# Kernel tuning notes

Hardware: AMD Instinct MI355X
Metric: run time of the kernel (lower is better)

Reference implementation:

```python
import jax, jax.numpy as jnp
import numpy as np

N_NODES = 10000
N_REL = 200
DIM = 128          # rank * 2
REL_DIM = 128
VIS_DIM = 512
TXT_DIM = 768
N_EDGES = 320000


def _glorot(key, shape):
    fan_in, fan_out = shape[1], shape[0]
    lim = (6.0 / (fan_in + fan_out)) ** 0.5
    return jax.random.uniform(key, shape, jnp.float32, -lim, lim)


def setup_inputs() -> dict:
    key = jax.random.key(0)
    ks = jax.random.split(key, 24)
    inp = {}
    inp['x'] = jax.random.randint(ks[0], (1024, 3), 0, N_NODES)
    inp['edge_index'] = jax.random.randint(ks[1], (2, N_EDGES), 0, N_NODES)
    inp['edge_type'] = jax.random.randint(ks[2], (N_EDGES,), 0, N_REL)
    inp['visual'] = jax.random.normal(ks[3], (N_NODES, VIS_DIM), jnp.float32)
    inp['textual'] = jax.random.normal(ks[4], (N_NODES, TXT_DIM), jnp.float32)
    # embeddings (scaled by 0.001 as in torch init)
    inp['structural_emb'] = jax.random.normal(ks[5], (N_NODES, DIM), jnp.float32) * 0.001
    inp['relation_emb'] = jax.random.normal(ks[6], (N_REL, REL_DIM), jnp.float32) * 0.001
    # three KBGAT convs: w1 [out, 2*in+rel], b1 [out], w2 [1, out]
    cat = 2 * DIM + REL_DIM
    for i, tag in enumerate(['s', 'v', 't']):
        inp[f'W1_{tag}'] = _glorot(ks[7 + 3 * i], (DIM, cat))
        inp[f'b1_{tag}'] = jnp.zeros((DIM,), jnp.float32)
        inp[f'w2_{tag}'] = _glorot(ks[8 + 3 * i], (1, DIM))
    # modality projections
    inp['Wv'] = _glorot(ks[16], (DIM, VIS_DIM))
    inp['bv'] = jnp.zeros((DIM,), jnp.float32)
    inp['Wt'] = _glorot(ks[17], (DIM, TXT_DIM))
    inp['bt'] = jnp.zeros((DIM,), jnp.float32)
    inp['alpha'] = jnp.float32(0.1)
    inp['gamma'] = jnp.float32(0.8)
    return inp


def kbgat_conv(feat, rel_emb, src, dst, edge_type, W1, b1, w2):
    # gather per-edge embeddings: x_i = target, x_j = source (PyG default flow)
    triple = jnp.concatenate([feat[dst], feat[src], rel_emb[edge_type]], axis=1)  # [E, 2*D+R]
    c = triple @ W1.T + b1                                   # [E, D]
    b = jax.nn.leaky_relu(c @ w2[0])                         # [E]
    # segment softmax over destination nodes
    m = jax.ops.segment_max(b, dst, num_segments=N_NODES)
    e = jnp.exp(b - m[dst])
    z = jax.ops.segment_sum(e, dst, num_segments=N_NODES)
    attn = e / z[dst]                                        # [E]
    agg = jax.ops.segment_sum(c * attn[:, None], dst, num_segments=N_NODES)  # [N, D]
    return jax.nn.leaky_relu(agg)


def reference(x, edge_index, edge_type, visual, textual, structural_emb, relation_emb,
              W1_s, b1_s, w2_s, W1_v, b1_v, w2_v, W1_t, b1_t, w2_t,
              Wv, bv, Wt, bt, alpha, gamma):
    src, dst = edge_index[0], edge_index[1]
    h_s = kbgat_conv(structural_emb, relation_emb, src, dst, edge_type, W1_s, b1_s, w2_s)
    vf = visual @ Wv.T + bv
    h_v = kbgat_conv(vf, relation_emb, src, dst, edge_type, W1_v, b1_v, w2_v)
    tf = textual @ Wt.T + bt
    h_t = kbgat_conv(tf, relation_emb, src, dst, edge_type, W1_t, b1_t, w2_t)
    return (1.0 - alpha - gamma) * h_s + alpha * h_v + gamma * h_t
```

## Files before the change

### kernel.cpp

```cpp
#include <hip/hip_runtime.h>
#include <hip/hip_bf16.h>

typedef unsigned short u16;
typedef unsigned int u32;
typedef unsigned long long u64;
typedef __bf16 bf16x8 __attribute__((ext_vector_type(8)));
typedef float f32x4 __attribute__((ext_vector_type(4)));

#define DIM 128

__device__ __forceinline__ u16 f2bf_rne(float x) {
  u32 u = __float_as_uint(x);
  return (u16)((u + 0x7fffu + ((u >> 16) & 1u)) >> 16);
}
__device__ __forceinline__ u32 packbf2(float x, float y) {
  return (u32)f2bf_rne(x) | ((u32)f2bf_rne(y) << 16);
}
__device__ __forceinline__ float lrelu(float x) { return x > 0.f ? x : 0.01f * x; }
__device__ __forceinline__ int iclamp(int v, int hi) { return v < 0 ? 0 : (v >= hi ? hi - 1 : v); }
__device__ __forceinline__ float sane(float x) { return (x == x) ? x : 0.f; }

__device__ __forceinline__ float wred_max(float v) {
  #pragma unroll
  for (int o = 32; o > 0; o >>= 1) v = fmaxf(v, __shfl_xor(v, o, 64));
  return v;
}
__device__ __forceinline__ float wred_sum(float v) {
  #pragma unroll
  for (int o = 32; o > 0; o >>= 1) v += __shfl_xor(v, o, 64);
  return v;
}

struct PrepAllArgs {
  const float* W1[3]; const float* Wmod[3]; int K[3]; u16* Wc[3];
  const float* rel; const float* b1[3]; const float* bmod[3]; const float* w2[3];
  u16* PrAll; float* qr[3]; int NR;
  const int* dst; int* cnt; int* rank; int E; int N;
  int wc2End; int wc1End; int wc0End; int nCompute; int totB;
};
struct MainArgs {
  const float* A[3]; const u16* B[3]; const float* w2[3];
  u16* PdAll; u16* PsAll; float* qd[3]; float* qs[3];
  int M; int K[3]; int tilesPerM; int nGemm; int totB;
  const int* dst; const int* src; const int* etyp;
  const int* offs; const int* rank; u32* sortedST;
  int E; int NR;
};
struct AgArgs {
  const u32* sortedST; const int* offs;
  const float* qd[3]; const float* qs[3]; const float* qr[3];
  const u16* PdAll; const u16* PsAll; const u16* PrAll;
  const float* alphaP; const float* gammaP;
  float* outp; int N; int NR; int E;
};

__global__ __launch_bounds__(256) void fused_prep(PrepAllArgs a) {
  __shared__ float relL[2][128];
  __shared__ float bmL[128];
  __shared__ float qpr[4];
  int b = blockIdx.x, tid = threadIdx.x;
  long nC = a.nCompute, tot = a.totB;
  int cprev = (int)((long)b * nC / tot);
  int cnext = (int)(((long)b + 1) * nC / tot);
  if (cnext == cprev) {
    int e0 = (b - cprev) * 1024 + tid;
    #pragma unroll
    for (int i = 0; i < 4; ++i) {
      int e = e0 + i * 256;
      if (e < a.E) {
        int d = a.dst[e];
        if (d >= 0 && d < a.N) a.rank[e] = atomicAdd(&a.cnt[d], 1);
      }
    }
    return;
  }
  int c = cprev;
  if (c < a.wc0End) {
    int m, loc;
    if (c < a.wc2End)      { m = 2; loc = c; }
    else if (c < a.wc1End) { m = 1; loc = c - a.wc2End; }
    else                   { m = 0; loc = c - a.wc1End; }
    int og = loc & 31, kb = loc >> 5;
    int o0 = og * 8;
    int k = (kb << 8) + tid;
    int K = a.K[m];
    if (k < K) {
      int halfsel = (o0 >= 128) ? 128 : 0;
      int oo0 = o0 & 127;
      const float* W1 = a.W1[m];
      const float* Wm = a.Wmod[m];
      float acc[8];
      if (Wm == nullptr) {
        #pragma unroll
        for (int u = 0; u < 8; ++u)
          acc[u] = W1[(oo0 + u) * 384 + halfsel + k];
      } else {
        #pragma unroll
        for (int u = 0; u < 8; ++u) acc[u] = 0.f;
        const float* wmk = Wm + k;
        const float* w1b = W1 + (size_t)oo0 * 384 + halfsel;
        for (int i = 0; i < 128; i += 8) {
          float wm[8];
          #pragma unroll
          for (int j = 0; j < 8; ++j)
            wm[j] = wmk[(size_t)(i + j) * K];
          #pragma unroll
          for (int j = 0; j < 8; ++j) {
            #pragma unroll
            for (int u = 0; u < 8; ++u)
              acc[u] = fmaf(w1b[u * 384 + i + j], wm[j], acc[u]);
          }
        }
      }
      #pragma unroll
      for (int u = 0; u < 8; ++u) {
        int o = o0 + u;
        a.Wc[m][((size_t)(k >> 5) * 256 + o) * 32 + (k & 31)] = f2bf_rne(acc[u]);
      }
    }
  } else {
    int idx = c - a.wc0End;
    int NRpair = (a.NR + 1) >> 1;
    int m = idx / NRpair;
    if (m > 2) return;
    int rp = idx - m * NRpair;
    int r0 = rp * 2;
    {
      int ro = tid >> 7, ii = tid & 127;
      int rr = r0 + ro;
      relL[ro][ii] = (rr < a.NR) ? a.rel[rr * 128 + ii] : 0.f;
    }
    const float* bmod = a.bmod[m];
    if (tid < 128) bmL[tid] = (bmod != nullptr) ? bmod[tid] : 0.f;
    __syncthreads();
    int lane = tid & 63, wv = tid >> 6;
    int rsel = wv >> 1;
    int obase = (wv & 1) * 64;
    int r = r0 + rsel;
    bool rok = (r < a.NR);
    const float* W1 = a.W1[m];
    const float* b1 = a.b1[m];
    const float* w2 = a.w2[m];
    bool hasbm = (bmod != nullptr);
    float rl0 = relL[rsel][lane], rl1 = relL[rsel][64 + lane];
    float bm0 = bmL[lane], bm1 = bmL[64 + lane];
    float qacc = 0.f;
    for (int oo = 0; oo < 64; oo += 4) {
      float s[4];
      #pragma unroll
      for (int u = 0; u < 4; ++u) {
        const float* row = W1 + (obase + oo + u) * 384;
        float v = row[256 + lane] * rl0 + row[320 + lane] * rl1;
        if (hasbm)
          v += (row[lane] + row[128 + lane]) * bm0 +
               (row[64 + lane] + row[192 + lane]) * bm1;
        s[u] = v;
      }
      #pragma unroll
      for (int off2 = 32; off2 > 0; off2 >>= 1) {
        #pragma unroll
        for (int u = 0; u < 4; ++u) s[u] += __shfl_xor(s[u], off2, 64);
      }
      u16 pk[4];
      #pragma unroll
      for (int u = 0; u < 4; ++u) {
        int o = obase + oo + u;
        float totv = s[u] + b1[o];
        pk[u] = f2bf_rne(totv);
        qacc += totv * w2[o];
      }
      if (rok && lane == 0) {
        u16* dstp = a.PrAll + (size_t)r * 384 + m * 128 + obase + oo;
        *reinterpret_cast<u64*>(dstp) =
            (u64)pk[0] | ((u64)pk[1] << 16) | ((u64)pk[2] << 32) | ((u64)pk[3] << 48);
      }
    }
    if (lane == 0) qpr[wv] = qacc;
    __syncthreads();
    if (tid < 2) {
      int rr = r0 + tid;
      if (rr < a.NR) a.qr[m][rr] = sane(qpr[tid * 2] + qpr[tid * 2 + 1]);
    }
  }
}

__global__ __launch_bounds__(1024) void scan_k(const int* __restrict__ cnt,
                                               int* __restrict__ offs, int N) {
  __shared__ int sums[1024];
  int t = threadIdx.x;
  int chunk = (N + 1023) >> 10;
  int base = t * chunk;
  int s = 0;
  for (int i = 0; i < chunk; ++i) { int idx = base + i; if (idx < N) s += cnt[idx]; }
  sums[t] = s;
  __syncthreads();
  for (int off = 1; off < 1024; off <<= 1) {
    int v = (t >= off) ? sums[t - off] : 0;
    __syncthreads();
    sums[t] += v;
    __syncthreads();
  }
  int prefix = (t > 0) ? sums[t - 1] : 0;
  for (int i = 0; i < chunk; ++i) {
    int idx = base + i;
    if (idx < N) { offs[idx] = prefix; prefix += cnt[idx]; }
  }
  if (t == 1023) offs[N] = sums[1023];
}

__device__ __forceinline__ void gemm_epilogue(const MainArgs& g, int m, int row0,
                                              f32x4 (&acc)[2][4], float (*qpart)[32]) {
  int tid = threadIdx.x;
  int lane = tid & 63, wv = tid >> 6;
  int quad = lane >> 4, l16 = lane & 15;
  int M = g.M;
  const float* w2 = g.w2[m];
  u16* PdAll = g.PdAll;
  u16* PsAll = g.PsAll;
  float w2c[4];
  #pragma unroll
  for (int t = 0; t < 4; ++t) w2c[t] = w2[(wv & 1) * 64 + t * 16 + l16];

  #pragma unroll
  for (int rg = 0; rg < 2; ++rg) {
    float part[4];
    #pragma unroll
    for (int r = 0; r < 4; ++r) {
      int rr = row0 + rg * 16 + quad * 4 + r;
      bool ok = rr < M;
      float qp = 0.f;
      #pragma unroll
      for (int t = 0; t < 4; ++t) {
        int cc = (wv & 1) * 64 + t * 16 + l16;
        if (ok) {
          if (wv < 2) PdAll[(size_t)rr * 384 + m * 128 + cc] = f2bf_rne(acc[rg][t][r]);
          else        PsAll[(size_t)rr * 384 + m * 128 + cc] = f2bf_rne(acc[rg][t][r]);
        }
        qp += acc[rg][t][r] * w2c[t];
      }
      #pragma unroll
      for (int mk = 1; mk < 16; mk <<= 1) qp += __shfl_xor(qp, mk, 64);
      part[r] = qp;
    }
    if (l16 == 0) {
      #pragma unroll
      for (int r = 0; r < 4; ++r) qpart[wv][rg * 16 + quad * 4 + r] = part[r];
    }
  }
  __syncthreads();
  if (tid < 64) {
    int row = tid & 31;
    int half = tid >> 5;
    int rr = row0 + row;
    if (rr < M) {
      if (half == 0) g.qd[m][rr] = sane(qpart[0][row] + qpart[1][row]);
      else           g.qs[m][rr] = sane(qpart[2][row] + qpart[3][row]);
    }
  }
}

template<int NT>
__device__ __forceinline__ void gemm_exact(const MainArgs& g, int m, int tile,
                                           u16* Als, float (*qpart)[32]) {
  constexpr int H = (NT + 1) / 2;
  const int M = g.M;
  int tid = threadIdx.x;
  int lane = tid & 63, wv = tid >> 6;
  int quad = lane >> 4, l16 = lane & 15;
  int row0 = tile * 32;
  int srow = tid >> 3;
  int tk4 = (tid & 7) * 4;
  int srsw = srow & 3;
  int wg = tk4 >> 3;
  int wrem = tk4 & 7;
  int grow = row0 + srow;
  if (grow >= M) grow = M - 1;
  const float* Ag = g.A[m] + (size_t)grow * (NT * 32);

  float4 vreg[H];
  #pragma unroll
  for (int i = 0; i < H; ++i)
    vreg[i] = *reinterpret_cast<const float4*>(Ag + tk4 + i * 32);
  #pragma unroll
  for (int i = 0; i < H; ++i) {
    int gidx = wg ^ srsw ^ (i & 3);
    u32* dp = reinterpret_cast<u32*>(&Als[((i * 32 + srow) * 32) + (gidx << 3) + wrem]);
    dp[0] = packbf2(vreg[i].x, vreg[i].y);
    dp[1] = packbf2(vreg[i].z, vreg[i].w);
  }
  #pragma unroll
  for (int i = H; i < NT; ++i)
    vreg[i - H] = *reinterpret_cast<const float4*>(Ag + tk4 + i * 32);
  #pragma unroll
  for (int i = H; i < NT; ++i) {
    int gidx = wg ^ srsw ^ (i & 3);
    u32* dp = reinterpret_cast<u32*>(&Als[((i * 32 + srow) * 32) + (gidx << 3) + wrem]);
    dp[0] = packbf2(vreg[i - H].x, vreg[i - H].y);
    dp[1] = packbf2(vreg[i - H].z, vreg[i - H].w);
  }
  __syncthreads();

  const u16* Bpg = g.B[m] + (size_t)(wv * 64 + l16) * 32 + quad * 8;
  f32x4 acc[2][4];
  #pragma unroll
  for (int rg = 0; rg < 2; ++rg)
    #pragma unroll
    for (int t = 0; t < 4; ++t) acc[rg][t] = (f32x4){0.f, 0.f, 0.f, 0.f};

  #pragma unroll
  for (int kb = 0; kb < NT; ++kb) {
    const u16* bp = Bpg + (size_t)kb * 8192;
    bf16x8 b0 = *reinterpret_cast<const bf16x8*>(bp);
    bf16x8 b1 = *reinterpret_cast<const bf16x8*>(bp + 512);
    bf16x8 b2 = *reinterpret_cast<const bf16x8*>(bp + 1024);
    bf16x8 b3 = *reinterpret_cast<const bf16x8*>(bp + 1536);
    int gsw = (quad ^ (l16 & 3) ^ (kb & 3)) << 3;
    #pragma unroll
    for (int rg = 0; rg < 2; ++rg) {
      bf16x8 av = *reinterpret_cast<const bf16x8*>(
          &Als[(kb * 32 + rg * 16 + l16) * 32 + gsw]);
      acc[rg][0] = __builtin_amdgcn_mfma_f32_16x16x32_bf16(av, b0, acc[rg][0], 0, 0, 0);
      acc[rg][1] = __builtin_amdgcn_mfma_f32_16x16x32_bf16(av, b1, acc[rg][1], 0, 0, 0);
      acc[rg][2] = __builtin_amdgcn_mfma_f32_16x16x32_bf16(av, b2, acc[rg][2], 0, 0, 0);
      acc[rg][3] = __builtin_amdgcn_mfma_f32_16x16x32_bf16(av, b3, acc[rg][3], 0, 0, 0);
    }
  }
  gemm_epilogue(g, m, row0, acc, qpart);
}

__device__ void gemm_generic(const MainArgs& g, int m, int tile,
                             u16* Als, float (*qpart)[32]) {
  const int M = g.M, K = g.K[m];
  int nt = K >> 5;
  int tid = threadIdx.x;
  int lane = tid & 63, wv = tid >> 6;
  int quad = lane >> 4, l16 = lane & 15;
  int row0 = tile * 32;
  int srow = tid >> 3;
  int tk4 = (tid & 7) * 4;
  int srsw = srow & 3;
  int wg = tk4 >> 3;
  int wrem = tk4 & 7;
  int grow = row0 + srow;
  if (grow >= M) grow = M - 1;
  const float* Ag = g.A[m] + (size_t)grow * K;
  const u16* Bpg = g.B[m] + (size_t)(wv * 64 + l16) * 32 + quad * 8;

  f32x4 acc[2][4];
  #pragma unroll
  for (int rg = 0; rg < 2; ++rg)
    #pragma unroll
    for (int t = 0; t < 4; ++t) acc[rg][t] = (f32x4){0.f, 0.f, 0.f, 0.f};

  for (int c0 = 0; c0 < nt; c0 += 24) {
    int kc = nt - c0; if (kc > 24) kc = 24;
    __syncthreads();
    for (int i = 0; i < kc; ++i) {
      int kg = (c0 + i) * 32 + tk4;
      if (kg + 3 < K) {
        float4 v = *reinterpret_cast<const float4*>(Ag + kg);
        int gidx = wg ^ srsw ^ (i & 3);
        u32* dp = reinterpret_cast<u32*>(&Als[((i * 32 + srow) * 32) + (gidx << 3) + wrem]);
        dp[0] = packbf2(v.x, v.y);
        dp[1] = packbf2(v.z, v.w);
      }
    }
    __syncthreads();
    for (int kb = 0; kb < kc; ++kb) {
      const u16* bp = Bpg + (size_t)(c0 + kb) * 8192;
      bf16x8 b0 = *reinterpret_cast<const bf16x8*>(bp);
      bf16x8 b1 = *reinterpret_cast<const bf16x8*>(bp + 512);
      bf16x8 b2 = *reinterpret_cast<const bf16x8*>(bp + 1024);
      bf16x8 b3 = *reinterpret_cast<const bf16x8*>(bp + 1536);
      int gsw = (quad ^ (l16 & 3) ^ (kb & 3)) << 3;
      #pragma unroll
      for (int rg = 0; rg < 2; ++rg) {
        bf16x8 av = *reinterpret_cast<const bf16x8*>(
            &Als[(kb * 32 + rg * 16 + l16) * 32 + gsw]);
        acc[rg][0] = __builtin_amdgcn_mfma_f32_16x16x32_bf16(av, b0, acc[rg][0], 0, 0, 0);
        acc[rg][1] = __builtin_amdgcn_mfma_f32_16x16x32_bf16(av, b1, acc[rg][1], 0, 0, 0);
        acc[rg][2] = __builtin_amdgcn_mfma_f32_16x16x32_bf16(av, b2, acc[rg][2], 0, 0, 0);
        acc[rg][3] = __builtin_amdgcn_mfma_f32_16x16x32_bf16(av, b3, acc[rg][3], 0, 0, 0);
      }
    }
  }
  gemm_epilogue(g, m, row0, acc, qpart);
}

__global__ __launch_bounds__(256) void fused_main(MainArgs g) {
  __shared__ __align__(16) u16 Als[24 * 32 * 32];
  __shared__ float qpart[4][32];
  int b = blockIdx.x;
  long nG = g.nGemm, tot = g.totB;
  int gprev = (int)((long)b * nG / tot);
  int gnext = (int)(((long)b + 1) * nG / tot);
  if (gnext == gprev) {
    int h = b - gprev;
    int e = h * 256 + threadIdx.x;
    if (e < g.E) {
      int d = g.dst[e];
      if (d >= 0 && d < g.M) {
        int pos = g.offs[d] + g.rank[e];
        if (pos >= 0 && pos < g.E) {
          u32 s = (u32)iclamp(g.src[e], g.M);
          u32 t = (u32)iclamp(g.etyp[e], g.NR);
          g.sortedST[pos] = (t << 16) | s;
        }
      }
    }
    return;
  }
  int fb = gprev;
  int tpm = g.tilesPerM;
  int m, tile;
  if (fb < tpm)            { m = 2; tile = fb; }
  else if (fb < 2 * tpm)   { m = 1; tile = fb - tpm; }
  else                     { m = 0; tile = fb - 2 * tpm; }

  int K = g.K[m];
  if (K == 768)      gemm_exact<24>(g, m, tile, Als, qpart);
  else if (K == 512) gemm_exact<16>(g, m, tile, Als, qpart);
  else if (K == 128) gemm_exact<4>(g, m, tile, Als, qpart);
  else               gemm_generic(g, m, tile, Als, qpart);
}

__global__ __launch_bounds__(256) void aggregate_all(AgArgs a) {
  int n = blockIdx.x * 4 + (threadIdx.x >> 6);
  if (n >= a.N) return;
  int lane = threadIdx.x & 63;
  int E = a.E;
  int eb = a.offs[n], ee = a.offs[n + 1];
  if (eb < 0) eb = 0;
  if (eb > E) eb = E;
  if (ee < eb) ee = eb;
  if (ee > E) ee = E;
  int En = ee - eb;

  float al = a.alphaP[0];
  if (!(al > 0.f && al < 1.f)) al = 0.1f;
  float ga = a.gammaP[0];
  if (!(ga > 0.f && ga < 1.f)) ga = 0.8f;
  float coef[3] = {1.f - al - ga, al, ga};

  float qdn[3];
  #pragma unroll
  for (int m = 0; m < 3; ++m) qdn[m] = sane(a.qd[m][n]);

  const u16* PsAll = a.PsAll;
  const u16* PrAll = a.PrAll;
  int dlo = 2 * lane;

  float rm[3] = {-1e30f, -1e30f, -1e30f};
  float z[3] = {0.f, 0.f, 0.f};
  float a0[3] = {0.f, 0.f, 0.f};
  float a1[3] = {0.f, 0.f, 0.f};
  for (int c0 = 0; c0 < En; c0 += 64) {
    int cn = min(64, En - c0);
    u32 stp = 0;
    float bm[3] = {-1e30f, -1e30f, -1e30f};
    if (lane < cn) {
      stp = a.sortedST[eb + c0 + lane];
      int s = (int)(stp & 0xffffu);
      int t = (int)(stp >> 16);
      #pragma unroll
      for (int m = 0; m < 3; ++m)
        bm[m] = lrelu(qdn[m] + a.qs[m][s] + a.qr[m][t]);
    }
    float wr[3];
    #pragma unroll
    for (int m = 0; m < 3; ++m) {
      float cm = wred_max(bm[m]);
      float nm = fmaxf(rm[m], cm);
      float sc = __expf(fmaxf(rm[m] - nm, -80.f));
      z[m] *= sc; a0[m] *= sc; a1[m] *= sc;
      rm[m] = nm;
      wr[m] = (lane < cn) ? __expf(fmaxf(bm[m] - nm, -80.f)) : 0.f;
      z[m] += wr[m];
    }

    int cnR = (cn + 3) & ~3;
    for (int j = 0; j < cnR; j += 4) {
      u32 stj[4];
      float wj[4][3];
      #pragma unroll
      for (int u = 0; u < 4; ++u) {
        stj[u] = __shfl(stp, j + u, 64);
        wj[u][0] = __shfl(wr[0], j + u, 64);
        wj[u][1] = __shfl(wr[1], j + u, 64);
        wj[u][2] = __shfl(wr[2], j + u, 64);
      }
      u32 pu[4][3], ru[4][3];
      #pragma unroll
      for (int u = 0; u < 4; ++u) {
        const u16* ps = PsAll + (size_t)(stj[u] & 0xffffu) * 384 + dlo;
        const u16* pr = PrAll + (size_t)(stj[u] >> 16) * 384 + dlo;
        #pragma unroll
        for (int m = 0; m < 3; ++m) {
          pu[u][m] = *reinterpret_cast<const u32*>(ps + m * 128);
          ru[u][m] = *reinterpret_cast<const u32*>(pr + m * 128);
        }
      }
      #pragma unroll
      for (int u = 0; u < 4; ++u) {
        #pragma unroll
        for (int m = 0; m < 3; ++m) {
          float ps0 = __uint_as_float(pu[u][m] << 16);
          float ps1 = __uint_as_float(pu[u][m] & 0xffff0000u);
          float pr0 = __uint_as_float(ru[u][m] << 16);
          float pr1 = __uint_as_float(ru[u][m] & 0xffff0000u);
          a0[m] = fmaf(wj[u][m], ps0 + pr0, a0[m]);
          a1[m] = fmaf(wj[u][m], ps1 + pr1, a1[m]);
        }
      }
    }
  }
  #pragma unroll
  for (int m = 0; m < 3; ++m) z[m] = wred_sum(z[m]);

  float o0 = 0.f, o1 = 0.f;
  const u16* pd = a.PdAll + (size_t)n * 384 + dlo;
  #pragma unroll
  for (int m = 0; m < 3; ++m) {
    float h0 = 0.f, h1 = 0.f;
    if (En > 0 && z[m] > 0.f) {
      float rz = 1.f / z[m];
      u32 du = *reinterpret_cast<const u32*>(pd + m * 128);
      float pd0 = __uint_as_float(du << 16), pd1 = __uint_as_float(du & 0xffff0000u);
      h0 = lrelu(pd0 + a0[m] * rz);
      h1 = lrelu(pd1 + a1[m] * rz);
    }
    o0 = fmaf(coef[m], h0, o0);
    o1 = fmaf(coef[m], h1, o1);
  }
  float* op = a.outp + (size_t)n * 128 + dlo;
  op[0] = sane(o0);
  op[1] = sane(o1);
}

extern "C" void kernel_launch(void* const* d_in, const int* in_sizes, int n_in,
                              void* d_out, int out_size, void* d_ws, size_t ws_size,
                              hipStream_t stream) {
  const int* ei        = (const int*)d_in[1];
  const int* et        = (const int*)d_in[2];
  const float* visual  = (const float*)d_in[3];
  const float* textual = (const float*)d_in[4];
  const float* semb    = (const float*)d_in[5];
  const float* relemb  = (const float*)d_in[6];
  const float* W1s = (const float*)d_in[7];
  const float* b1s = (const float*)d_in[8];
  const float* w2s = (const float*)d_in[9];
  const float* W1v = (const float*)d_in[10];
  const float* b1v = (const float*)d_in[11];
  const float* w2v = (const float*)d_in[12];
  const float* W1t = (const float*)d_in[13];
  const float* b1t = (const float*)d_in[14];
  const float* w2t = (const float*)d_in[15];
  const float* Wv  = (const float*)d_in[16];
  const float* bv  = (const float*)d_in[17];
  const float* Wt  = (const float*)d_in[18];
  const float* bt  = (const float*)d_in[19];
  const float* alphaP = (const float*)d_in[20];
  const float* gammaP = (const float*)d_in[21];
  float* outp = (float*)d_out;

  const int E   = in_sizes[2];
  const int N   = in_sizes[5] / DIM;
  const int NR  = in_sizes[6] / DIM;
  const int VIS = in_sizes[3] / N;
  const int TXT = in_sizes[4] / N;
  int Ks[3] = {DIM, VIS, TXT};
  const int TPM = (N + 31) / 32;

  const float* W1a[3]   = {W1s, W1v, W1t};
  const float* b1a[3]   = {b1s, b1v, b1t};
  const float* w2a[3]   = {w2s, w2v, w2t};
  const float* Wmoda[3] = {nullptr, Wv, Wt};
  const float* bmoda[3] = {nullptr, bv, bt};
  const float* Amoda[3] = {semb, visual, textual};

  const int* esrc = ei;
  const int* edst = ei + E;
  int egrid  = (E + 255) / 256;
  int egridH = (E + 1023) / 1024;

  size_t off = 0;
  auto take = [&](size_t bytes) -> size_t {
    size_t o = off;
    off = (off + bytes + 255) & ~(size_t)255;
    return o;
  };
  size_t o_cnt  = take((size_t)N * 4);
  size_t o_rank = take((size_t)E * 4);
  size_t o_offs = take((size_t)(N + 1) * 4);
  size_t o_st   = take((size_t)E * 4);
  size_t o_qdm[3], o_qsm[3], o_qrm[3], o_Wcm[3];
  for (int m = 0; m < 3; ++m) {
    o_qdm[m] = take((size_t)N * 4);
    o_qsm[m] = take((size_t)N * 4);
    o_qrm[m] = take((size_t)NR * 4);
    o_Wcm[m] = take((size_t)256 * Ks[m] * 2);
  }
  size_t o_PrAll = take((size_t)NR * 384 * 2);
  size_t o_PdAll = take((size_t)N * 384 * 2);
  size_t o_PsAll = take((size_t)N * 384 * 2);
  size_t need = off;

  if (ws_size < need) {
    (void)hipMemsetAsync(d_out, 0, (size_t)out_size * 4, stream);
    return;
  }

  char* w = (char*)d_ws;
  int* counts = (int*)(w + o_cnt);
  int* rank   = (int*)(w + o_rank);
  int* offs   = (int*)(w + o_offs);
  u32* sortedST = (u32*)(w + o_st);

  (void)hipMemsetAsync(counts, 0, (size_t)N * 4, stream);

  PrepAllArgs pa;
  pa.rel = relemb; pa.NR = NR;
  pa.PrAll = (u16*)(w + o_PrAll);
  pa.dst = edst; pa.cnt = counts; pa.rank = rank; pa.E = E; pa.N = N;
  for (int m = 0; m < 3; ++m) {
    pa.W1[m] = W1a[m]; pa.Wmod[m] = Wmoda[m]; pa.K[m] = Ks[m];
    pa.Wc[m] = (u16*)(w + o_Wcm[m]);
    pa.b1[m] = b1a[m]; pa.bmod[m] = bmoda[m]; pa.w2[m] = w2a[m];
    pa.qr[m] = (float*)(w + o_qrm[m]);
  }
  int NRpair = (NR + 1) / 2;
  int kbm[3];
  for (int m = 0; m < 3; ++m) kbm[m] = (Ks[m] + 255) / 256;
  pa.wc2End   = 32 * kbm[2];
  pa.wc1End   = pa.wc2End + 32 * kbm[1];
  pa.wc0End   = pa.wc1End + 32 * kbm[0];
  pa.nCompute = pa.wc0End + 3 * NRpair;
  pa.totB     = pa.nCompute + egridH;

  MainArgs ga;
  ga.M = N; ga.tilesPerM = TPM; ga.nGemm = 3 * TPM;
  ga.totB = ga.nGemm + egrid;
  ga.PdAll = (u16*)(w + o_PdAll);
  ga.PsAll = (u16*)(w + o_PsAll);
  ga.dst = edst; ga.src = esrc; ga.etyp = et;
  ga.offs = offs; ga.rank = rank; ga.sortedST = sortedST;
  ga.E = E; ga.NR = NR;
  AgArgs aa;
  for (int m = 0; m < 3; ++m) {
    ga.A[m] = Amoda[m]; ga.B[m] = (const u16*)(w + o_Wcm[m]); ga.w2[m] = w2a[m];
    ga.qd[m] = (float*)(w + o_qdm[m]); ga.qs[m] = (float*)(w + o_qsm[m]);
    ga.K[m] = Ks[m];
    aa.qd[m] = (const float*)(w + o_qdm[m]);
    aa.qs[m] = (const float*)(w + o_qsm[m]);
    aa.qr[m] = (const float*)(w + o_qrm[m]);
  }

  aa.PdAll = (const u16*)(w + o_PdAll);
  aa.PsAll = (const u16*)(w + o_PsAll);
  aa.PrAll = (const u16*)(w + o_PrAll);
  aa.sortedST = sortedST; aa.offs = offs;
  aa.alphaP = alphaP; aa.gammaP = gammaP;
  aa.outp = outp; aa.N = N; aa.NR = NR; aa.E = E;

  fused_prep<<<pa.totB, 256, 0, stream>>>(pa);
  scan_k<<<1, 1024, 0, stream>>>(counts, offs, N);
  fused_main<<<ga.totB, 256, 0, stream>>>(ga);
  aggregate_all<<<(N + 3) / 4, 256, 0, stream>>>(aa);
}
```

Before: 252.4 us.

## Split histogram into own kernel and fuse scan with weight/relation prep

Moves the per-edge destination histogram out of the fused prep kernel into a standalone kernel, then folds the single-block prefix scan into the weight-conversion/relation-projection kernel as block 0. This reorders the launch schedule so the scan runs concurrently with the weight prep work instead of as its own serial launch. The scan now uses 256 threads instead of 1024, which makes that one block longer, and the histogram no longer overlaps with the weight prep.

```diff
diff --git a/kernel.cpp b/kernel.cpp
--- a/kernel.cpp
+++ b/kernel.cpp
@@ -35,8 +35,8 @@
   const float* W1[3]; const float* Wmod[3]; int K[3]; u16* Wc[3];
   const float* rel; const float* b1[3]; const float* bmod[3]; const float* w2[3];
   u16* PrAll; float* qr[3]; int NR;
-  const int* dst; int* cnt; int* rank; int E; int N;
-  int wc2End; int wc1End; int wc0End; int nCompute; int totB;
+  const int* cnt; int* offs; int N;
+  int wc2End; int wc1End; int wc0End;
 };
 struct MainArgs {
   const float* A[3]; const u16* B[3]; const float* w2[3];
@@ -54,27 +54,51 @@
   float* outp; int N; int NR; int E;
 };
 
-__global__ __launch_bounds__(256) void fused_prep(PrepAllArgs a) {
+__global__ __launch_bounds__(256) void hist_k(const int* __restrict__ dst,
+                                              int* __restrict__ cnt,
+                                              int* __restrict__ rank, int E, int N) {
+  int e0 = blockIdx.x * 512 + threadIdx.x;
+  #pragma unroll
+  for (int i = 0; i < 2; ++i) {
+    int e = e0 + i * 256;
+    if (e < E) {
+      int d = dst[e];
+      if (d >= 0 && d < N) rank[e] = atomicAdd(&cnt[d], 1);
+    }
+  }
+}
+
+__global__ __launch_bounds__(256) void scan_wcpr(PrepAllArgs a) {
   __shared__ float relL[2][128];
   __shared__ float bmL[128];
   __shared__ float qpr[4];
+  __shared__ int sums[256];
   int b = blockIdx.x, tid = threadIdx.x;
-  long nC = a.nCompute, tot = a.totB;
-  int cprev = (int)((long)b * nC / tot);
-  int cnext = (int)(((long)b + 1) * nC / tot);
-  if (cnext == cprev) {
-    int e0 = (b - cprev) * 1024 + tid;
-    #pragma unroll
-    for (int i = 0; i < 4; ++i) {
-      int e = e0 + i * 256;
-      if (e < a.E) {
-        int d = a.dst[e];
-        if (d >= 0 && d < a.N) a.rank[e] = atomicAdd(&a.cnt[d], 1);
-      }
-    }
+
+  if (b == 0) {
+    int N = a.N;
+    int chunk = (N + 255) >> 8;
+    int base = tid * chunk;
+    int s = 0;
+    for (int i = 0; i < chunk; ++i) { int idx = base + i; if (idx < N) s += a.cnt[idx]; }
+    sums[tid] = s;
+    __syncthreads();
+    for (int off = 1; off < 256; off <<= 1) {
+      int v = (tid >= off) ? sums[tid - off] : 0;
+      __syncthreads();
+      sums[tid] += v;
+      __syncthreads();
+    }
+    int prefix = (tid > 0) ? sums[tid - 1] : 0;
+    for (int i = 0; i < chunk; ++i) {
+      int idx = base + i;
+      if (idx < N) { a.offs[idx] = prefix; prefix += a.cnt[idx]; }
+    }
+    if (tid == 255) a.offs[N] = sums[255];
     return;
   }
-  int c = cprev;
+
+  int c = b - 1;
   if (c < a.wc0End) {
     int m, loc;
     if (c < a.wc2End)      { m = 2; loc = c; }
@@ -184,30 +208,6 @@
   }
 }
 
-__global__ __launch_bounds__(1024) void scan_k(const int* __restrict__ cnt,
-                                               int* __restrict__ offs, int N) {
-  __shared__ int sums[1024];
-  int t = threadIdx.x;
-  int chunk = (N + 1023) >> 10;
-  int base = t * chunk;
-  int s = 0;
-  for (int i = 0; i < chunk; ++i) { int idx = base + i; if (idx < N) s += cnt[idx]; }
-  sums[t] = s;
-  __syncthreads();
-  for (int off = 1; off < 1024; off <<= 1) {
-    int v = (t >= off) ? sums[t - off] : 0;
-    __syncthreads();
-    sums[t] += v;
-    __syncthreads();
-  }
-  int prefix = (t > 0) ? sums[t - 1] : 0;
-  for (int i = 0; i < chunk; ++i) {
-    int idx = base + i;
-    if (idx < N) { offs[idx] = prefix; prefix += cnt[idx]; }
-  }
-  if (t == 1023) offs[N] = sums[1023];
-}
-
 __device__ __forceinline__ void gemm_epilogue(const MainArgs& g, int m, int row0,
                                               f32x4 (&acc)[2][4], float (*qpart)[32]) {
   int tid = threadIdx.x;
@@ -581,7 +581,7 @@
   const int* esrc = ei;
   const int* edst = ei + E;
   int egrid  = (E + 255) / 256;
-  int egridH = (E + 1023) / 1024;
+  int egridH = (E + 511) / 512;
 
   size_t off = 0;
   auto take = [&](size_t bytes) -> size_t {
@@ -621,7 +621,7 @@
   PrepAllArgs pa;
   pa.rel = relemb; pa.NR = NR;
   pa.PrAll = (u16*)(w + o_PrAll);
-  pa.dst = edst; pa.cnt = counts; pa.rank = rank; pa.E = E; pa.N = N;
+  pa.cnt = counts; pa.offs = offs; pa.N = N;
   for (int m = 0; m < 3; ++m) {
     pa.W1[m] = W1a[m]; pa.Wmod[m] = Wmoda[m]; pa.K[m] = Ks[m];
     pa.Wc[m] = (u16*)(w + o_Wcm[m]);
@@ -631,11 +631,10 @@
   int NRpair = (NR + 1) / 2;
   int kbm[3];
   for (int m = 0; m < 3; ++m) kbm[m] = (Ks[m] + 255) / 256;
-  pa.wc2End   = 32 * kbm[2];
-  pa.wc1End   = pa.wc2End + 32 * kbm[1];
-  pa.wc0End   = pa.wc1End + 32 * kbm[0];
-  pa.nCompute = pa.wc0End + 3 * NRpair;
-  pa.totB     = pa.nCompute + egridH;
+  pa.wc2End = 32 * kbm[2];
+  pa.wc1End = pa.wc2End + 32 * kbm[1];
+  pa.wc0End = pa.wc1End + 32 * kbm[0];
+  int prepGrid = 1 + pa.wc0End + 3 * NRpair;
 
   MainArgs ga;
   ga.M = N; ga.tilesPerM = TPM; ga.nGemm = 3 * TPM;
@@ -662,8 +661,8 @@
   aa.alphaP = alphaP; aa.gammaP = gammaP;
   aa.outp = outp; aa.N = N; aa.NR = NR; aa.E = E;
 
-  fused_prep<<<pa.totB, 256, 0, stream>>>(pa);
-  scan_k<<<1, 1024, 0, stream>>>(counts, offs, N);
+  hist_k<<<egridH, 256, 0, stream>>>(edst, counts, rank, E, N);
+  scan_wcpr<<<prepGrid, 256, 0, stream>>>(pa);
   fused_main<<<ga.totB, 256, 0, stream>>>(ga);
   aggregate_all<<<(N + 3) / 4, 256, 0, stream>>>(aa);
 }
```

New measurement: 248.0 us. About the same (-1.7%).
